# Kernel optimization log

Hardware: AMD Instinct MI355X
Metric: run time of the kernel (lower is better)

The kernel has to match this reference:

```python
import jax, jax.numpy as jnp
import numpy as np

NUM_HEADS = 16


def setup_inputs() -> dict:
    key = jax.random.key(0)
    ks = jax.random.split(key, 7)
    T, B, E = 2048, 2, 1024
    return {
        "query": jax.random.normal(ks[0], (T, B, E), jnp.float32),
        "key": jax.random.normal(ks[1], (T, B, E), jnp.float32),
        "value": jax.random.normal(ks[2], (T, B, E), jnp.float32),
        "query_pos": jax.random.normal(ks[3], (T, B, E), jnp.float32),
        "key_pos": jax.random.normal(ks[4], (T, B, E), jnp.float32),
        "W": jax.random.normal(ks[5], (E, E), jnp.float32) * (1.0 / np.sqrt(E)),
        "b": jax.random.normal(ks[6], (E,), jnp.float32) * 0.01,
    }


def reference(query, key, value, query_pos, key_pos, W, b):
    T, B, E = query.shape
    S = key.shape[0]
    H = NUM_HEADS
    D = E // H
    scale = jnp.asarray(D ** 0.5, query.dtype)

    identity = query  # residual uses query BEFORE positional add
    q = query + query_pos
    k = key + key_pos

    # (T,B,E) -> (B,H,T,D)
    q = q.reshape(T, B, H, D).transpose(1, 2, 0, 3)
    k = k.reshape(S, B, H, D).transpose(1, 2, 0, 3)
    v = value.reshape(S, B, H, D).transpose(1, 2, 0, 3)

    attn = jnp.einsum("bhtd,bhsd->bhts", q, k) / scale
    attn = jax.nn.softmax(attn, axis=-1)  # dropout p=0 -> identity

    out = jnp.einsum("bhts,bhsd->bhtd", attn, v)
    out = out.transpose(2, 0, 1, 3).reshape(T, B, E)  # (B,H,T,D)->(T,B,E)
    out = out @ W.T + b  # fuse_heads linear; out_dropout p=0 -> identity
    out = out + identity

    attn_avg = attn.sum(axis=1) / H  # average over heads -> (B,T,S)
    return out, attn_avg
```

## Files before the change

kernel.cpp:

```cpp
#include <hip/hip_runtime.h>

#define T_DIM 2048
#define S_DIM 2048
#define B_DIM 2
#define E_DIM 1024
#define H_DIM 16
#define D_DIM 64
#define MSHIFT 20.0f
#define EXP2S 0.18033688f
#define EXP2C -28.8539008f
#define EXP2(x) __builtin_amdgcn_exp2f(x)

typedef unsigned short u16;
typedef unsigned int u32;
typedef float v4f __attribute__((ext_vector_type(4)));
typedef short v8s __attribute__((ext_vector_type(8)));

__device__ __forceinline__ u16 f2bf(float f) {
    union { float f; u32 u; } x; x.f = f;
    return (u16)((x.u + 0x7fffu + ((x.u >> 16) & 1u)) >> 16);
}
__device__ __forceinline__ u16 f2bfr(float f) {
    union { float f; u32 u; } x; x.f = f;
    return (u16)((x.u + 0x8000u) >> 16);
}
__device__ __forceinline__ v4f mfma16(v8s a, v8s b, v4f c) {
    return __builtin_amdgcn_mfma_f32_16x16x32_bf16(a, b, c, 0, 0, 0);
}
__device__ __forceinline__ v8s ld8(const u16* p) {
    return *reinterpret_cast<const v8s*>(p);
}

__global__ __launch_bounds__(256) void prep_qk(
    const float* __restrict__ q, const float* __restrict__ qp,
    const float* __restrict__ k, const float* __restrict__ kp,
    u16* __restrict__ qb, u16* __restrict__ ks) {
    int o = blockIdx.x * 256 + threadIdx.x;
    int d = o & 63, t = (o >> 6) & 2047, h = (o >> 17) & 15, b = o >> 21;
    int src = ((t * B_DIM + b) << 10) + (h << 6) + d;
    qb[o] = f2bf(q[src] + qp[src]);
    ks[o] = f2bf(k[src] + kp[src]);
}

__global__ __launch_bounds__(256) void prep_w(const float* __restrict__ W, u16* __restrict__ Wb) {
    int o = blockIdx.x * 256 + threadIdx.x;
    Wb[o] = f2bf(W[o]);
}

__global__ __launch_bounds__(256) void prep_vt(const float* __restrict__ V, u16* __restrict__ vt) {
    __shared__ float tile[64 * 65];
    int bx = blockIdx.x;
    int bh = bx >> 5;
    int s0 = (bx & 31) * 64;
    int b = bh >> 4, h = bh & 15;
    int tid = threadIdx.x;
    int quarter = tid >> 6, c = tid & 63;
    int boff = b * E_DIM + h * 64;
#pragma unroll
    for (int p = 0; p < 16; ++p) {
        int r = quarter * 16 + p;
        tile[r * 65 + c] = V[(size_t)(s0 + r) * (B_DIM * E_DIM) + boff + c];
    }
    __syncthreads();
#pragma unroll
    for (int p = 0; p < 16; ++p) {
        int d = quarter * 16 + p;
        vt[(size_t)bh * (D_DIM * S_DIM) + (size_t)d * S_DIM + s0 + c] = f2bf(tile[c * 65 + d]);
    }
}

#define PITCH 72
__global__ __launch_bounds__(256) void attn_pv(
    const u16* __restrict__ qb, const u16* __restrict__ ks, const u16* __restrict__ vt,
    float* __restrict__ lin, u16* __restrict__ Xb) {
    __shared__ u16 Kl[2][64 * PITCH];
    __shared__ u16 Vl[2][64 * PITCH];
    __shared__ u16 Pl[4][32 * PITCH];

    int bx = blockIdx.x;
    int bh = bx >> 4;
    int b = bh >> 4, h = bh & 15;
    int tid = threadIdx.x;
    int w = tid >> 6;
    int tbase = (bx & 15) * 128 + w * 32;
    int lane = tid & 63;
    int m = lane & 15, g = lane >> 4;

    int srow = tid >> 2;
    int sqtr = (tid & 3) * 16;

    uint4 kr0, kr1, vr0, vr1;
    auto load_stage = [&](int s0) {
        const uint4* kp = reinterpret_cast<const uint4*>(
            ks + ((size_t)bh * S_DIM + s0 + srow) * 64 + sqtr);
        kr0 = kp[0]; kr1 = kp[1];
        const uint4* vp = reinterpret_cast<const uint4*>(
            vt + (size_t)bh * (D_DIM * S_DIM) + (size_t)srow * S_DIM + s0 + sqtr);
        vr0 = vp[0]; vr1 = vp[1];
    };
    auto write_stage = [&](int buf) {
        uint4* kd = reinterpret_cast<uint4*>(&Kl[buf][srow * PITCH + sqtr]);
        kd[0] = kr0; kd[1] = kr1;
        uint4* vd = reinterpret_cast<uint4*>(&Vl[buf][srow * PITCH + sqtr]);
        vd[0] = vr0; vd[1] = vr1;
    };

    const u16* qrow = qb + ((size_t)bh * T_DIM + tbase + m) * 64 + g * 8;
    v8s aq[2][2];
    aq[0][0] = ld8(qrow);        aq[0][1] = ld8(qrow + 32);
    aq[1][0] = ld8(qrow + 1024); aq[1][1] = ld8(qrow + 1024 + 32);

    v4f O[2][4];
    float lacc[2][4];
#pragma unroll
    for (int tr = 0; tr < 2; ++tr) {
#pragma unroll
        for (int dd = 0; dd < 4; ++dd) O[tr][dd] = (v4f){0.f, 0.f, 0.f, 0.f};
#pragma unroll
        for (int r = 0; r < 4; ++r) lacc[tr][r] = 0.f;
    }

    load_stage(0);
    write_stage(0);
    load_stage(64);
    __syncthreads();

    u16* Pw = Pl[w];
    for (int it = 0; it < 32; ++it) {
        int buf = it & 1;
        const u16* Kb = Kl[buf];
        const u16* Vb = Vl[buf];
#pragma unroll
        for (int ss = 0; ss < 4; ++ss) {
            v8s kf0 = ld8(&Kb[(ss * 16 + m) * PITCH + g * 8]);
            v8s kf1 = ld8(&Kb[(ss * 16 + m) * PITCH + 32 + g * 8]);
#pragma unroll
            for (int tr = 0; tr < 2; ++tr) {
                v4f z = {0.f, 0.f, 0.f, 0.f};
                z = mfma16(aq[tr][0], kf0, z);
                z = mfma16(aq[tr][1], kf1, z);
#pragma unroll
                for (int r = 0; r < 4; ++r) {
                    float e = EXP2(fmaf(z[r], EXP2S, EXP2C));
                    lacc[tr][r] += e;
                    Pw[(tr * 16 + g * 4 + r) * PITCH + ss * 16 + m] = f2bfr(e);
                }
            }
        }
        v8s ap[2][2];
#pragma unroll
        for (int tr = 0; tr < 2; ++tr) {
            ap[tr][0] = ld8(&Pw[(tr * 16 + m) * PITCH + g * 8]);
            ap[tr][1] = ld8(&Pw[(tr * 16 + m) * PITCH + 32 + g * 8]);
        }
#pragma unroll
        for (int dd = 0; dd < 4; ++dd) {
            v8s bv0 = ld8(&Vb[(dd * 16 + m) * PITCH + g * 8]);
            v8s bv1 = ld8(&Vb[(dd * 16 + m) * PITCH + 32 + g * 8]);
#pragma unroll
            for (int tr = 0; tr < 2; ++tr) {
                O[tr][dd] = mfma16(ap[tr][0], bv0, O[tr][dd]);
                O[tr][dd] = mfma16(ap[tr][1], bv1, O[tr][dd]);
            }
        }
        if (it + 1 < 32) {
            write_stage(buf ^ 1);
            if (it + 2 < 32) load_stage((it + 2) * 64);
        }
        __syncthreads();
    }

#pragma unroll
    for (int tr = 0; tr < 2; ++tr)
#pragma unroll
        for (int r = 0; r < 4; ++r) {
#pragma unroll
            for (int off = 1; off <= 8; off <<= 1)
                lacc[tr][r] += __shfl_xor(lacc[tr][r], off);
        }

#pragma unroll
    for (int tr = 0; tr < 2; ++tr)
#pragma unroll
        for (int r = 0; r < 4; ++r) {
            float linv = 1.0f / lacc[tr][r];
            int t = tbase + tr * 16 + g * 4 + r;
            if (m == 0) lin[(size_t)bh * T_DIM + t] = linv;
#pragma unroll
            for (int dd = 0; dd < 4; ++dd)
                Xb[((size_t)t * B_DIM + b) * E_DIM + h * 64 + dd * 16 + m] =
                    f2bf(O[tr][dd][r] * linv);
        }
}

__global__ __launch_bounds__(256, 4) void attn_avg(
    const u16* __restrict__ qb, const u16* __restrict__ ks,
    const float* __restrict__ lin, float* __restrict__ out1) {
    __shared__ u16 Kl[2][64 * PITCH];
    int bx = blockIdx.x;
    int b = bx >> 9;
    int tt = (bx >> 5) & 15;
    int st = bx & 31;
    int tid = threadIdx.x;
    int w = tid >> 6;
    int tbase = tt * 128 + w * 32;
    int sbase = st * 64;
    int lane = tid & 63, m = lane & 15, g = lane >> 4;

    int srow = tid >> 2;
    int sqtr = (tid & 3) * 16;

    uint4 kr0, kr1;
    auto load_stage = [&](int h) {
        const uint4* kp = reinterpret_cast<const uint4*>(
            ks + ((size_t)(b * 16 + h) * S_DIM + sbase + srow) * 64 + sqtr);
        kr0 = kp[0]; kr1 = kp[1];
    };
    auto write_stage = [&](int buf) {
        uint4* kd = reinterpret_cast<uint4*>(&Kl[buf][srow * PITCH + sqtr]);
        kd[0] = kr0; kd[1] = kr1;
    };

    v8s aqc00, aqc01, aqc10, aqc11, aqn00, aqn01, aqn10, aqn11;
    float livc[2][4], livn[2][4];
    auto load_q = [&](int h, v8s& a00, v8s& a01, v8s& a10, v8s& a11, float (&liv)[2][4]) {
        int bh = b * 16 + h;
        const u16* qrow = qb + ((size_t)bh * T_DIM + tbase + m) * 64 + g * 8;
        a00 = ld8(qrow);        a01 = ld8(qrow + 32);
        a10 = ld8(qrow + 1024); a11 = ld8(qrow + 1024 + 32);
#pragma unroll
        for (int tr = 0; tr < 2; ++tr)
#pragma unroll
            for (int r = 0; r < 4; ++r)
                liv[tr][r] = lin[(size_t)bh * T_DIM + tbase + tr * 16 + g * 4 + r] * (1.0f / 16.0f);
    };

    v4f AVG[2][4];
#pragma unroll
    for (int tr = 0; tr < 2; ++tr)
#pragma unroll
        for (int ss = 0; ss < 4; ++ss) AVG[tr][ss] = (v4f){0.f, 0.f, 0.f, 0.f};

    load_stage(0);
    write_stage(0);
    load_stage(1);
    load_q(0, aqc00, aqc01, aqc10, aqc11, livc);
    __syncthreads();

    for (int h = 0; h < H_DIM; ++h) {
        int buf = h & 1;
        if (h + 1 < H_DIM) load_q(h + 1, aqn00, aqn01, aqn10, aqn11, livn);

        const u16* Kb = Kl[buf];
#pragma unroll
        for (int ss = 0; ss < 4; ++ss) {
            v8s kf0 = ld8(&Kb[(ss * 16 + m) * PITCH + g * 8]);
            v8s kf1 = ld8(&Kb[(ss * 16 + m) * PITCH + 32 + g * 8]);
            {
                v4f z = {0.f, 0.f, 0.f, 0.f};
                z = mfma16(aqc00, kf0, z);
                z = mfma16(aqc01, kf1, z);
#pragma unroll
                for (int r = 0; r < 4; ++r)
                    AVG[0][ss][r] += EXP2(fmaf(z[r], EXP2S, EXP2C)) * livc[0][r];
            }
            {
                v4f z = {0.f, 0.f, 0.f, 0.f};
                z = mfma16(aqc10, kf0, z);
                z = mfma16(aqc11, kf1, z);
#pragma unroll
                for (int r = 0; r < 4; ++r)
                    AVG[1][ss][r] += EXP2(fmaf(z[r], EXP2S, EXP2C)) * livc[1][r];
            }
        }
        if (h + 1 < H_DIM) {
            write_stage(buf ^ 1);
            if (h + 2 < H_DIM) load_stage(h + 2);
        }
        __syncthreads();
        aqc00 = aqn00; aqc01 = aqn01; aqc10 = aqn10; aqc11 = aqn11;
#pragma unroll
        for (int tr = 0; tr < 2; ++tr)
#pragma unroll
            for (int r = 0; r < 4; ++r) livc[tr][r] = livn[tr][r];
    }
#pragma unroll
    for (int tr = 0; tr < 2; ++tr)
#pragma unroll
        for (int ss = 0; ss < 4; ++ss)
#pragma unroll
            for (int r = 0; r < 4; ++r) {
                int t = tbase + tr * 16 + g * 4 + r;
                out1[((size_t)b * T_DIM + t) * S_DIM + sbase + ss * 16 + m] = AVG[tr][ss][r];
            }
}

__global__ __launch_bounds__(256) void linear_mfma(
    const u16* __restrict__ Xb, const u16* __restrict__ Wb,
    const float* __restrict__ bias, const float* __restrict__ query,
    float* __restrict__ out0) {
    __shared__ u16 Al[2][64 * PITCH];
    __shared__ u16 Wl[2][128 * PITCH];
    int bx = blockIdx.x;
    int it = bx >> 3, jt = bx & 7;
    int tid = threadIdx.x;
    int w = tid >> 6;
    int lane = tid & 63;
    int m = lane & 15, g = lane >> 4;

    int arow = tid >> 2, aq4 = (tid & 3) * 16;
    int wrow = tid >> 1, wh2 = (tid & 1) * 32;

    uint4 ar0, ar1, wr0, wr1, wr2, wr3;
    auto load_stage = [&](int k0) {
        const uint4* ap = reinterpret_cast<const uint4*>(
            Xb + (size_t)(it * 64 + arow) * E_DIM + k0 + aq4);
        ar0 = ap[0]; ar1 = ap[1];
        const uint4* wp = reinterpret_cast<const uint4*>(
            Wb + (size_t)(jt * 128 + wrow) * E_DIM + k0 + wh2);
        wr0 = wp[0]; wr1 = wp[1]; wr2 = wp[2]; wr3 = wp[3];
    };
    auto write_stage = [&](int buf) {
        uint4* ad = reinterpret_cast<uint4*>(&Al[buf][arow * PITCH + aq4]);
        ad[0] = ar0; ad[1] = ar1;
        uint4* wd = reinterpret_cast<uint4*>(&Wl[buf][wrow * PITCH + wh2]);
        wd[0] = wr0; wd[1] = wr1; wd[2] = wr2; wd[3] = wr3;
    };

    v4f acc[4][2];
#pragma unroll
    for (int tr = 0; tr < 4; ++tr)
#pragma unroll
        for (int nn = 0; nn < 2; ++nn) acc[tr][nn] = (v4f){0.f, 0.f, 0.f, 0.f};

    load_stage(0);
    write_stage(0);
    load_stage(64);
    __syncthreads();

    for (int itk = 0; itk < 16; ++itk) {
        int buf = itk & 1;
        const u16* Ab = Al[buf];
        const u16* Ws = Wl[buf];
        v8s af[4][2], wf[2][2];
#pragma unroll
        for (int tr = 0; tr < 4; ++tr) {
            af[tr][0] = ld8(&Ab[(tr * 16 + m) * PITCH + g * 8]);
            af[tr][1] = ld8(&Ab[(tr * 16 + m) * PITCH + 32 + g * 8]);
        }
#pragma unroll
        for (int nn = 0; nn < 2; ++nn) {
            wf[nn][0] = ld8(&Ws[((w * 2 + nn) * 16 + m) * PITCH + g * 8]);
            wf[nn][1] = ld8(&Ws[((w * 2 + nn) * 16 + m) * PITCH + 32 + g * 8]);
        }
#pragma unroll
        for (int tr = 0; tr < 4; ++tr)
#pragma unroll
            for (int nn = 0; nn < 2; ++nn) {
                acc[tr][nn] = mfma16(af[tr][0], wf[nn][0], acc[tr][nn]);
                acc[tr][nn] = mfma16(af[tr][1], wf[nn][1], acc[tr][nn]);
            }
        if (itk + 1 < 16) {
            write_stage(buf ^ 1);
            if (itk + 2 < 16) load_stage((itk + 2) * 64);
        }
        __syncthreads();
    }

#pragma unroll
    for (int tr = 0; tr < 4; ++tr)
#pragma unroll
        for (int nn = 0; nn < 2; ++nn) {
            int col = jt * 128 + (w * 2 + nn) * 16 + m;
            float bv = bias[col];
#pragma unroll
            for (int r = 0; r < 4; ++r) {
                int row = it * 64 + tr * 16 + g * 4 + r;
                out0[(size_t)row * E_DIM + col] =
                    acc[tr][nn][r] + bv + query[(size_t)row * E_DIM + col];
            }
        }
}

extern "C" void kernel_launch(void* const* d_in, const int* in_sizes, int n_in,
                              void* d_out, int out_size, void* d_ws, size_t ws_size,
                              hipStream_t stream) {
    const float* query = (const float*)d_in[0];
    const float* key   = (const float*)d_in[1];
    const float* value = (const float*)d_in[2];
    const float* qpos  = (const float*)d_in[3];
    const float* kpos  = (const float*)d_in[4];
    const float* W     = (const float*)d_in[5];
    const float* bias  = (const float*)d_in[6];

    char* ws = (char*)d_ws;
    u16*   qb  = (u16*)(ws);
    u16*   ks  = (u16*)(ws + (size_t)( 8u << 20));
    u16*   vt  = (u16*)(ws + (size_t)(16u << 20));
    u16*   Wb  = (u16*)(ws + (size_t)(24u << 20));
    float* lin = (float*)(ws + (size_t)(26u << 20));
    u16*   Xb  = (u16*)(ws + (size_t)(27u << 20));

    float* out0 = (float*)d_out;
    float* out1 = out0 + (size_t)T_DIM * B_DIM * E_DIM;

    prep_qk<<<(B_DIM * H_DIM * T_DIM * D_DIM) / 256, 256, 0, stream>>>(query, qpos, key, kpos, qb, ks);
    prep_w<<<(E_DIM * E_DIM) / 256, 256, 0, stream>>>(W, Wb);
    prep_vt<<<B_DIM * H_DIM * (S_DIM / 64), 256, 0, stream>>>(value, vt);
    attn_pv<<<B_DIM * H_DIM * (T_DIM / 128), 256, 0, stream>>>(qb, ks, vt, lin, Xb);
    attn_avg<<<B_DIM * (T_DIM / 128) * (S_DIM / 64), 256, 0, stream>>>(qb, ks, lin, out1);
    linear_mfma<<<(T_DIM * B_DIM / 64) * (E_DIM / 128), 256, 0, stream>>>(Xb, Wb, bias, query, out0);
}
```

Before: 266.2 us.

## Keep softmax probabilities in registers by computing S^T and feeding PV MFMA directly

```diff
diff --git a/kernel.cpp b/kernel.cpp
--- a/kernel.cpp
+++ b/kernel.cpp
@@ -6,7 +6,6 @@
 #define E_DIM 1024
 #define H_DIM 16
 #define D_DIM 64
-#define MSHIFT 20.0f
 #define EXP2S 0.18033688f
 #define EXP2C -28.8539008f
 #define EXP2(x) __builtin_amdgcn_exp2f(x)
@@ -15,17 +14,21 @@
 typedef unsigned int u32;
 typedef float v4f __attribute__((ext_vector_type(4)));
 typedef short v8s __attribute__((ext_vector_type(8)));
+typedef short v4s __attribute__((ext_vector_type(4)));
 
 __device__ __forceinline__ u16 f2bf(float f) {
     union { float f; u32 u; } x; x.f = f;
     return (u16)((x.u + 0x7fffu + ((x.u >> 16) & 1u)) >> 16);
 }
-__device__ __forceinline__ u16 f2bfr(float f) {
-    union { float f; u32 u; } x; x.f = f;
-    return (u16)((x.u + 0x8000u) >> 16);
+__device__ __forceinline__ u32 pk2(float lo, float hi) {
+    union { float f; u32 u; } a, b; a.f = lo; b.f = hi;
+    return ((a.u + 0x8000u) >> 16) | (((b.u + 0x8000u) >> 16) << 16);
 }
 __device__ __forceinline__ v4f mfma16(v8s a, v8s b, v4f c) {
     return __builtin_amdgcn_mfma_f32_16x16x32_bf16(a, b, c, 0, 0, 0);
+}
+__device__ __forceinline__ v4f mfma16x16(v4s a, v4s b, v4f c) {
+    return __builtin_amdgcn_mfma_f32_16x16x16bf16_1k(a, b, c, 0, 0, 0);
 }
 __device__ __forceinline__ v8s ld8(const u16* p) {
     return *reinterpret_cast<const v8s*>(p);
@@ -75,7 +78,6 @@
     float* __restrict__ lin, u16* __restrict__ Xb) {
     __shared__ u16 Kl[2][64 * PITCH];
     __shared__ u16 Vl[2][64 * PITCH];
-    __shared__ u16 Pl[4][32 * PITCH];
 
     int bx = blockIdx.x;
     int bh = bx >> 4;
@@ -111,21 +113,17 @@
     aq[1][0] = ld8(qrow + 1024); aq[1][1] = ld8(qrow + 1024 + 32);
 
     v4f O[2][4];
-    float lacc[2][4];
-#pragma unroll
-    for (int tr = 0; tr < 2; ++tr) {
+    float lacc[2] = {0.f, 0.f};
+#pragma unroll
+    for (int tr = 0; tr < 2; ++tr)
 #pragma unroll
         for (int dd = 0; dd < 4; ++dd) O[tr][dd] = (v4f){0.f, 0.f, 0.f, 0.f};
-#pragma unroll
-        for (int r = 0; r < 4; ++r) lacc[tr][r] = 0.f;
-    }
 
     load_stage(0);
     write_stage(0);
     load_stage(64);
     __syncthreads();
 
-    u16* Pw = Pl[w];
     for (int it = 0; it < 32; ++it) {
         int buf = it & 1;
         const u16* Kb = Kl[buf];
@@ -134,33 +132,41 @@
         for (int ss = 0; ss < 4; ++ss) {
             v8s kf0 = ld8(&Kb[(ss * 16 + m) * PITCH + g * 8]);
             v8s kf1 = ld8(&Kb[(ss * 16 + m) * PITCH + 32 + g * 8]);
-#pragma unroll
-            for (int tr = 0; tr < 2; ++tr) {
+            v4s pa0, pa1;
+            {
                 v4f z = {0.f, 0.f, 0.f, 0.f};
-                z = mfma16(aq[tr][0], kf0, z);
-                z = mfma16(aq[tr][1], kf1, z);
-#pragma unroll
-                for (int r = 0; r < 4; ++r) {
-                    float e = EXP2(fmaf(z[r], EXP2S, EXP2C));
-                    lacc[tr][r] += e;
-                    Pw[(tr * 16 + g * 4 + r) * PITCH + ss * 16 + m] = f2bfr(e);
-                }
-            }
-        }
-        v8s ap[2][2];
-#pragma unroll
-        for (int tr = 0; tr < 2; ++tr) {
-            ap[tr][0] = ld8(&Pw[(tr * 16 + m) * PITCH + g * 8]);
-            ap[tr][1] = ld8(&Pw[(tr * 16 + m) * PITCH + 32 + g * 8]);
-        }
-#pragma unroll
-        for (int dd = 0; dd < 4; ++dd) {
-            v8s bv0 = ld8(&Vb[(dd * 16 + m) * PITCH + g * 8]);
-            v8s bv1 = ld8(&Vb[(dd * 16 + m) * PITCH + 32 + g * 8]);
-#pragma unroll
-            for (int tr = 0; tr < 2; ++tr) {
-                O[tr][dd] = mfma16(ap[tr][0], bv0, O[tr][dd]);
-                O[tr][dd] = mfma16(ap[tr][1], bv1, O[tr][dd]);
+                z = mfma16(kf0, aq[0][0], z);
+                z = mfma16(kf1, aq[0][1], z);
+                float e0 = EXP2(fmaf(z[0], EXP2S, EXP2C));
+                float e1 = EXP2(fmaf(z[1], EXP2S, EXP2C));
+                float e2 = EXP2(fmaf(z[2], EXP2S, EXP2C));
+                float e3 = EXP2(fmaf(z[3], EXP2S, EXP2C));
+                lacc[0] += (e0 + e1) + (e2 + e3);
+                union { u32 u[2]; v4s s; } pk_;
+                pk_.u[0] = pk2(e0, e1);
+                pk_.u[1] = pk2(e2, e3);
+                pa0 = pk_.s;
+            }
+            {
+                v4f z = {0.f, 0.f, 0.f, 0.f};
+                z = mfma16(kf0, aq[1][0], z);
+                z = mfma16(kf1, aq[1][1], z);
+                float e0 = EXP2(fmaf(z[0], EXP2S, EXP2C));
+                float e1 = EXP2(fmaf(z[1], EXP2S, EXP2C));
+                float e2 = EXP2(fmaf(z[2], EXP2S, EXP2C));
+                float e3 = EXP2(fmaf(z[3], EXP2S, EXP2C));
+                lacc[1] += (e0 + e1) + (e2 + e3);
+                union { u32 u[2]; v4s s; } pk_;
+                pk_.u[0] = pk2(e0, e1);
+                pk_.u[1] = pk2(e2, e3);
+                pa1 = pk_.s;
+            }
+#pragma unroll
+            for (int dd = 0; dd < 4; ++dd) {
+                v4s bv = *reinterpret_cast<const v4s*>(
+                    &Vb[(dd * 16 + m) * PITCH + ss * 16 + g * 4]);
+                O[0][dd] = mfma16x16(pa0, bv, O[0][dd]);
+                O[1][dd] = mfma16x16(pa1, bv, O[1][dd]);
             }
         }
         if (it + 1 < 32) {
@@ -171,26 +177,21 @@
     }
 
 #pragma unroll
-    for (int tr = 0; tr < 2; ++tr)
+    for (int tr = 0; tr < 2; ++tr) {
+        lacc[tr] += __shfl_xor(lacc[tr], 16);
+        lacc[tr] += __shfl_xor(lacc[tr], 32);
+        float linv = 1.0f / lacc[tr];
+        if (lane < 16) lin[(size_t)bh * T_DIM + tbase + tr * 16 + m] = linv;
 #pragma unroll
         for (int r = 0; r < 4; ++r) {
-#pragma unroll
-            for (int off = 1; off <= 8; off <<= 1)
-                lacc[tr][r] += __shfl_xor(lacc[tr][r], off);
-        }
-
-#pragma unroll
-    for (int tr = 0; tr < 2; ++tr)
-#pragma unroll
-        for (int r = 0; r < 4; ++r) {
-            float linv = 1.0f / lacc[tr][r];
+            float lr = __shfl(linv, g * 4 + r);
             int t = tbase + tr * 16 + g * 4 + r;
-            if (m == 0) lin[(size_t)bh * T_DIM + t] = linv;
 #pragma unroll
             for (int dd = 0; dd < 4; ++dd)
                 Xb[((size_t)t * B_DIM + b) * E_DIM + h * 64 + dd * 16 + m] =
-                    f2bf(O[tr][dd][r] * linv);
-        }
+                    f2bf(O[tr][dd][r] * lr);
+        }
+    }
 }
 
 __global__ __launch_bounds__(256, 4) void attn_avg(
```

Result: no change. 268.4 us (+0.8%).
